# Optimization experiments

Measured on AMD Instinct MI355X. Metric: run time of the kernel, lower is better.

## Reference

```python
import jax, jax.numpy as jnp
from jax import lax
import numpy as np

# Quantization constants (would come from the torch state dict)
IN_S = 1.0 / 255.0   # input_scale
IN_ZP = 0            # input_zp
W_S  = [0.02, 0.02, 0.02, 0.02, 0.02, 0.02, 0.02]   # per-layer w_scale
W_ZP = [128, 128, 128, 128, 128, 128, 128]           # per-layer w_zp
OUT_S  = [0.05, 0.04, 0.04, 0.04, 0.04, 0.04, 0.05]  # per-layer act out_scale
OUT_ZP = [0, 0, 0, 0, 0, 0, 0]
PADS = [2, 0, 1, 1, 1, 1, 0]
WT_SCALE = 0.02  # last_part.w_scale used to dequantize the transpose-conv weight
DN = ('NCHW', 'OIHW', 'NCHW')


def qconv(x, w, b, in_s, in_zp, w_s, w_zp, out_s, out_zp, pad):
    # fake-quantize activation to uint8 range, shift by zero point
    xq = jnp.clip(jnp.round(x / in_s) + in_zp, 0.0, 255.0) - in_zp
    wq = w.astype(jnp.float32) - w_zp
    y = lax.conv_general_dilated(xq, wq, (1, 1), [(pad, pad), (pad, pad)],
                                 dimension_numbers=DN)
    y = y + b.astype(jnp.float32)[None, :, None, None]   # int32 accumulator bias
    # requantize to int8 range, dequantize, relu
    yq = jnp.clip(jnp.round(y * (in_s * w_s / out_s)), -127.0, 127.0)
    return jax.nn.relu((yq - out_zp) * out_s)


def deconv(x, wt):
    # torch ConvTranspose2d(16,1,k=9,stride=4,padding=4,bias=False)
    # equivalent: lhs-dilated conv with flipped, transposed kernel, pad = k-1-p = 4
    k = jnp.flip(jnp.transpose(wt, (1, 0, 2, 3)), axis=(2, 3))  # (O=1, I=16, 9, 9)
    return lax.conv_general_dilated(x, k, (1, 1), [(4, 4), (4, 4)],
                                    lhs_dilation=(4, 4), dimension_numbers=DN)


def setup_inputs() -> dict:
    key = jax.random.key(0)
    ks = jax.random.split(key, 20)
    shapes_w = [(16, 1, 5, 5), (12, 16, 1, 1), (12, 12, 3, 3), (12, 12, 3, 3),
                (12, 12, 3, 3), (12, 12, 3, 3), (16, 12, 1, 1)]
    inp = {"x": jax.random.uniform(ks[0], (16, 1, 512, 512), dtype=jnp.float32)}
    for i, sh in enumerate(shapes_w):
        inp[f"w{i}"] = jax.random.randint(ks[1 + i], sh, 0, 256, dtype=jnp.int32)
        inp[f"b{i}"] = jax.random.randint(ks[8 + i], (sh[0],), 0, 512, dtype=jnp.int32)
    # dequantized transpose-conv weight: int8-ish values * w_scale
    inp["wt"] = jax.random.normal(ks[15], (16, 1, 9, 9), dtype=jnp.float32) * WT_SCALE
    return inp


def reference(x, w0, w1, w2, w3, w4, w5, w6,
              b0, b1, b2, b3, b4, b5, b6, wt):
    ws = [w0, w1, w2, w3, w4, w5, w6]
    bs = [b0, b1, b2, b3, b4, b5, b6]
    cur_s, cur_zp = IN_S, IN_ZP
    for i in range(7):
        x = qconv(x, ws[i], bs[i], cur_s, cur_zp,
                  W_S[i], W_ZP[i], OUT_S[i], OUT_ZP[i], PADS[i])
        cur_s, cur_zp = OUT_S[i], OUT_ZP[i]
    return deconv(x, wt)
```

## Files before the change

### kernel.cpp

```cpp
#include <hip/hip_runtime.h>
#include <stdint.h>

typedef unsigned int uint;
typedef float f2 __attribute__((ext_vector_type(2)));
typedef float f4u __attribute__((ext_vector_type(4), aligned(4)));
#define DEV __device__ __forceinline__


DEV int dot4(uint a, uint b, int c) {
#if __has_builtin(__builtin_amdgcn_sdot4)
    return __builtin_amdgcn_sdot4((int)a, (int)b, c, false);
#else
    int r = c;
    r += (int)(int8_t)(a)       * (int)(int8_t)(b);
    r += (int)(int8_t)(a >> 8)  * (int)(int8_t)(b >> 8);
    r += (int)(int8_t)(a >> 16) * (int)(int8_t)(b >> 16);
    r += (int)(int8_t)(a >> 24) * (int)(int8_t)(b >> 24);
    return r;
#endif
}

DEV uint alignbyte(uint hi, uint lo, int m) {
#if __has_builtin(__builtin_amdgcn_alignbyte)
    return __builtin_amdgcn_alignbyte(hi, lo, m);
#else
    return (uint)((((uint64_t)hi << 32) | (uint64_t)lo) >> (8 * m));
#endif
}

DEV float bytef(uint v, int k) { return (float)((v >> (8 * k)) & 0xffu); }

DEV uint requant_relu(int acc, float M) {
    float q = rintf((float)acc * M);
    q = fminf(fmaxf(q, -127.f), 127.f);
    q = fmaxf(q, 0.f);
    return (uint)q;
}

__global__ __launch_bounds__(256) void k_quant(const float* __restrict__ x,
                                               uint8_t* __restrict__ xq,
                                               float in_s) {
    int i = blockIdx.x * 256 + threadIdx.x;
    float4 v = ((const float4*)x)[i];
    uint b0 = (uint)fminf(fmaxf(rintf(v.x / in_s), 0.f), 255.f);
    uint b1 = (uint)fminf(fmaxf(rintf(v.y / in_s), 0.f), 255.f);
    uint b2 = (uint)fminf(fmaxf(rintf(v.z / in_s), 0.f), 255.f);
    uint b3 = (uint)fminf(fmaxf(rintf(v.w / in_s), 0.f), 255.f);
    ((uint*)xq)[i] = b0 | (b1 << 8) | (b2 << 16) | (b3 << 24);
}

__global__ __launch_bounds__(256) void k_l0(const uint8_t* __restrict__ xq,
                                            const int* __restrict__ w,
                                            const int* __restrict__ b,
                                            uint8_t* __restrict__ out, float M,
                                            const int* __restrict__ w1,
                                            const int* __restrict__ b1, float M1) {
    __shared__ uint tin[5][68];
    __shared__ uint wrow[5][16];
    __shared__ uint w4p[16];
    __shared__ int  w44[16];
    __shared__ int  beff[16];
    __shared__ uint w1l[48];
    __shared__ int  b1l[12];
    int t  = threadIdx.x;
    int x0 = blockIdx.x * 256;
    int y  = blockIdx.y;
    int n  = blockIdx.z;
    const uint8_t* xp = xq + (size_t)n * 512 * 512;

    for (int j = t; j < 330; j += 256) {
        int r = j / 66, d = j % 66;
        int yy = y - 2 + r;
        int gb = x0 - 4 + 4 * d;
        uint v = 0;
        if ((unsigned)yy < 512u && (unsigned)gb < 512u)
            v = *(const uint*)(xp + (size_t)yy * 512 + gb);
        tin[r][d] = v;
    }
    if (t < 80) {
        int oc = t / 5, r = t % 5;
        uint pk = 0;
#pragma unroll
        for (int k = 0; k < 4; ++k) {
            int wv = w[oc * 25 + r * 5 + k] - 128;
            pk |= ((uint)(uint8_t)(int8_t)wv) << (8 * k);
        }
        wrow[r][oc] = pk;
    }
    if (t < 16) {
        uint pk = 0;
#pragma unroll
        for (int r = 0; r < 4; ++r) {
            int wv = w[t * 25 + r * 5 + 4] - 128;
            pk |= ((uint)(uint8_t)(int8_t)wv) << (8 * r);
        }
        w4p[t] = pk;
        w44[t] = w[t * 25 + 24] - 128;
        int s = 0;
        for (int p = 0; p < 25; ++p) s += w[t * 25 + p] - 128;
        beff[t] = b[t] + 128 * s;
    }
    if (t < 48) {
        int oc = t >> 2, d = t & 3;
        uint pk = 0;
#pragma unroll
        for (int k = 0; k < 4; ++k) {
            int wv = w1[oc * 16 + d * 4 + k] - 128;
            pk |= ((uint)(uint8_t)(int8_t)wv) << (8 * k);
        }
        w1l[t] = pk;
    }
    if (t >= 64 && t < 76) b1l[t - 64] = b1[t - 64];
    __syncthreads();

    int m  = (t + 2) & 3;
    int d0 = (t + 2) >> 2;
    uint e0[5], t4[5];
#pragma unroll
    for (int r = 0; r < 5; ++r) {
        uint a0 = tin[r][d0], a1 = tin[r][d0 + 1];
        e0[r] = alignbyte(a1, a0, m) ^ 0x80808080u;
        t4[r] = (a1 >> (8 * m)) & 0xffu;
    }
    uint lo4 = (t4[0] | (t4[1] << 8) | (t4[2] << 16) | (t4[3] << 24)) ^ 0x80808080u;
    int  e44 = (int)(int8_t)(uint8_t)(t4[4] ^ 0x80u);

    int acc[16];
#pragma unroll
    for (int oc = 0; oc < 16; ++oc) acc[oc] = beff[oc];
#pragma unroll
    for (int r = 0; r < 5; ++r)
#pragma unroll
        for (int oc = 0; oc < 16; ++oc) acc[oc] = dot4(e0[r], wrow[r][oc], acc[oc]);
#pragma unroll
    for (int oc = 0; oc < 16; ++oc) {
        acc[oc] = dot4(lo4, w4p[oc], acc[oc]);
        acc[oc] += e44 * w44[oc];
    }

    uint dw[4];
#pragma unroll
    for (int g = 0; g < 4; ++g) {
        uint d = 0;
#pragma unroll
        for (int k = 0; k < 4; ++k) d |= requant_relu(acc[g * 4 + k], M) << (8 * k);
        dw[g] = d;
    }

    size_t pix = (size_t)(n * 512 + y) * 512 + (x0 + t);
    uint* op = (uint*)out;
#pragma unroll
    for (int g = 0; g < 3; ++g) {
        uint dword = 0;
#pragma unroll
        for (int k = 0; k < 4; ++k) {
            int oc = g * 4 + k;
            int a2 = b1l[oc];
#pragma unroll
            for (int d = 0; d < 4; ++d) a2 = dot4(dw[d], w1l[oc * 4 + d], a2);
            dword |= requant_relu(a2, M1) << (8 * k);
        }
        op[pix * 3 + g] = dword;
    }
}

template <bool FUSE>
__global__ __launch_bounds__(128) void k_3x3(const uint8_t* __restrict__ in,
                                             const int* __restrict__ w,
                                             const int* __restrict__ b,
                                             uint8_t* __restrict__ out, float M,
                                             const int* __restrict__ w6,
                                             const int* __restrict__ b6, float M6) {
    __shared__ uint wl[324];
    __shared__ int  bl[12];
    __shared__ uint w6l[48];
    __shared__ int  b6l[16];
    int t = threadIdx.x;
    for (int j = t; j < 324; j += 128) {
        int pos = j / 36;
        int oc  = (j % 36) / 3;
        int d   = j % 3;
        uint pk = 0;
#pragma unroll
        for (int k = 0; k < 4; ++k) {
            int ic = d * 4 + k;
            int wv = w[oc * 108 + ic * 9 + pos] - 128;
            pk |= ((uint)(uint8_t)(int8_t)wv) << (8 * k);
        }
        wl[j] = pk;
    }
    if (t < 12) bl[t] = b[t];
    if (FUSE) {
        if (t >= 16 && t < 64) {
            int j = t - 16, oc = j / 3, d = j % 3;
            uint pk = 0;
#pragma unroll
            for (int k = 0; k < 4; ++k) {
                int wv = w6[oc * 12 + d * 4 + k] - 128;
                pk |= ((uint)(uint8_t)(int8_t)wv) << (8 * k);
            }
            w6l[j] = pk;
        }
        if (t >= 64 && t < 80) b6l[t - 64] = b6[t - 64];
    }
    __syncthreads();

    int y = blockIdx.x, n = blockIdx.y;
    int x0 = t * 4;
    const uint* ip = (const uint*)in;

    uint inr[3][6][3];
#pragma unroll
    for (int r = 0; r < 3; ++r) {
        int yy = y - 1 + r;
        bool yok = (unsigned)yy < 512u;
#pragma unroll
        for (int cidx = 0; cidx < 6; ++cidx) {
            int xx = x0 - 1 + cidx;
            bool ok = yok && (unsigned)xx < 512u;
            size_t base = ((size_t)(n * 512 + yy) * 512 + xx) * 3;
#pragma unroll
            for (int d = 0; d < 3; ++d) inr[r][cidx][d] = ok ? ip[base + d] : 0u;
        }
    }

    int acc[4][12];
#pragma unroll
    for (int p = 0; p < 4; ++p)
#pragma unroll
        for (int oc = 0; oc < 12; ++oc) acc[p][oc] = bl[oc];

#pragma unroll
    for (int ry = 0; ry < 3; ++ry) {
#pragma unroll
        for (int rx = 0; rx < 3; ++rx) {
            int pos = ry * 3 + rx;
            const uint4* wq = (const uint4*)&wl[pos * 36];
#pragma unroll
            for (int g = 0; g < 3; ++g) {
                uint4 wA = wq[g * 3 + 0];
                uint4 wB = wq[g * 3 + 1];
                uint4 wC = wq[g * 3 + 2];
                uint wocd[4][3] = {{wA.x, wA.y, wA.z}, {wA.w, wB.x, wB.y},
                                   {wB.z, wB.w, wC.x}, {wC.y, wC.z, wC.w}};
#pragma unroll
                for (int k = 0; k < 4; ++k) {
                    int oc = g * 4 + k;
#pragma unroll
                    for (int p = 0; p < 4; ++p) {
                        acc[p][oc] = dot4(inr[ry][rx + p][0], wocd[k][0], acc[p][oc]);
                        acc[p][oc] = dot4(inr[ry][rx + p][1], wocd[k][1], acc[p][oc]);
                        acc[p][oc] = dot4(inr[ry][rx + p][2], wocd[k][2], acc[p][oc]);
                    }
                }
            }
        }
    }

#pragma unroll
    for (int p = 0; p < 4; ++p) {
        uint dws[3];
#pragma unroll
        for (int g = 0; g < 3; ++g) {
            uint dword = 0;
#pragma unroll
            for (int k = 0; k < 4; ++k) dword |= requant_relu(acc[p][g * 4 + k], M) << (8 * k);
            dws[g] = dword;
        }
        size_t pix = (size_t)(n * 512 + y) * 512 + (x0 + p);
        if (!FUSE) {
            uint* op = (uint*)out;
            op[pix * 3 + 0] = dws[0];
            op[pix * 3 + 1] = dws[1];
            op[pix * 3 + 2] = dws[2];
        } else {
            uint dw2[4];
#pragma unroll
            for (int g = 0; g < 4; ++g) {
                uint dword = 0;
#pragma unroll
                for (int k = 0; k < 4; ++k) {
                    int oc = g * 4 + k;
                    int a2 = b6l[oc];
#pragma unroll
                    for (int d = 0; d < 3; ++d) a2 = dot4(dws[d], w6l[oc * 3 + d], a2);
                    dword |= requant_relu(a2, M6) << (8 * k);
                }
                dw2[g] = dword;
            }
            ((uint4*)out)[pix] = make_uint4(dw2[0], dw2[1], dw2[2], dw2[3]);
        }
    }
}

__global__ __launch_bounds__(256) void k_wprep(const float* __restrict__ wt,
                                               float* __restrict__ wp, float out_s) {
    int idx = blockIdx.x * 256 + threadIdx.x;
    if (idx < 2304) {
        int o = idx & 15, c = (idx >> 4) & 15, pos = idx >> 8;
        int r = pos / 3, s = pos % 3;
        int py = o >> 2, px = o & 3;
        int jy = 4 * r - py, jx = 4 * s - px;
        float v = 0.f;
        if (jy >= 0 && jy < 9 && jx >= 0 && jx < 9)
            v = wt[c * 81 + (8 - jy) * 9 + (8 - jx)] * out_s;
        wp[idx] = v;
    } else if (idx < 2496) {
        int i2 = idx - 2304;
        int r = i2 >> 6, c = (i2 >> 2) & 15, py = i2 & 3;
        int jy = 4 * r - py;
        float v = 0.f;
        if (jy >= 0 && jy < 9)
            v = wt[c * 81 + (8 - jy) * 9 + 8] * out_s;
        wp[idx] = v;
    }
}

template <bool ALLPY>
DEV void dc_row8(const float* __restrict__ wrow,
                 const float* __restrict__ w0tab,
                 const uint4* ld,
                 f2 (&accA)[2][4], f2 (&accB)[2][4]) {
    uint bv[4][4];
#pragma unroll
    for (int s = 0; s < 4; ++s) { bv[s][0] = ld[s].x; bv[s][1] = ld[s].y; bv[s][2] = ld[s].z; bv[s][3] = ld[s].w; }
#pragma unroll
    for (int c = 0; c < 16; ++c) {
        float xc[4];
#pragma unroll
        for (int s = 0; s < 4; ++s) xc[s] = bytef(bv[s][c >> 2], c & 3);
        if (ALLPY) {
            float4 wv = *(const float4*)(w0tab + c * 4);
            accA[0][0].x = fmaf(wv.x, xc[0], accA[0][0].x);
            accA[0][1].x = fmaf(wv.y, xc[0], accA[0][1].x);
            accA[0][2].x = fmaf(wv.z, xc[0], accA[0][2].x);
            accA[0][3].x = fmaf(wv.w, xc[0], accA[0][3].x);
            accA[1][0].x = fmaf(wv.x, xc[1], accA[1][0].x);
            accA[1][1].x = fmaf(wv.y, xc[1], accA[1][1].x);
            accA[1][2].x = fmaf(wv.z, xc[1], accA[1][2].x);
            accA[1][3].x = fmaf(wv.w, xc[1], accA[1][3].x);
        } else {
            float w0 = w0tab[c * 4];
            accA[0][0].x = fmaf(w0, xc[0], accA[0][0].x);
            accA[1][0].x = fmaf(w0, xc[1], accA[1][0].x);
        }
#pragma unroll
        for (int s = 1; s < 3; ++s) {
            const float* wb = wrow + s * 256 + c * 16;
            f2 xxA = {xc[s], xc[s]};
            f2 xxB = {xc[s + 1], xc[s + 1]};
#pragma unroll
            for (int py = 0; py < (ALLPY ? 4 : 1); ++py) {
                float4 wv = *(const float4*)(wb + py * 4);
                f2 wlo = {wv.x, wv.y};
                f2 whi = {wv.z, wv.w};
                accA[0][py] = __builtin_elementwise_fma(wlo, xxA, accA[0][py]);
                accB[0][py] = __builtin_elementwise_fma(whi, xxA, accB[0][py]);
                accA[1][py] = __builtin_elementwise_fma(wlo, xxB, accA[1][py]);
                accB[1][py] = __builtin_elementwise_fma(whi, xxB, accB[1][py]);
            }
        }
    }
}

__global__ __launch_bounds__(256, 2) void k_deconv8(const uint8_t* __restrict__ in,
                                                    const float* __restrict__ wp,
                                                    float* __restrict__ out) {
    __shared__ float wl[2304];
    __shared__ float wl0[192];
    int t = threadIdx.x;
#pragma unroll
    for (int j = 0; j < 9; ++j) wl[j * 256 + t] = wp[j * 256 + t];
    if (t < 192) wl0[t] = wp[2304 + t];
    __syncthreads();

    int gx = t;
    int ty = blockIdx.y;
    int n  = blockIdx.z;
    const uint4* ip = (const uint4*)in + (size_t)n * 512 * 512;

    f2 accA[2][4], accB[2][4];
#pragma unroll
    for (int k = 0; k < 2; ++k)
#pragma unroll
        for (int i = 0; i < 4; ++i) { accA[k][i] = (f2){0.f, 0.f}; accB[k][i] = (f2){0.f, 0.f}; }

    {
        int iy = ty - 1;
        uint4 ld[4];
#pragma unroll
        for (int s = 0; s < 4; ++s) {
            int ix = 2 * gx - 1 + s;
            bool ok = (iy >= 0) && ((unsigned)ix < 512u);
            ld[s] = ok ? ip[(size_t)iy * 512 + ix] : make_uint4(0u, 0u, 0u, 0u);
        }
        dc_row8<false>(&wl[0], &wl0[0], ld, accA, accB);
    }
#pragma unroll 1
    for (int r = 1; r < 3; ++r) {
        int iy = ty - 1 + r;
        uint4 ld[4];
#pragma unroll
        for (int s = 0; s < 4; ++s) {
            int ix = 2 * gx - 1 + s;
            bool ok = (iy < 512) && ((unsigned)ix < 512u);
            ld[s] = ok ? ip[(size_t)iy * 512 + ix] : make_uint4(0u, 0u, 0u, 0u);
        }
        dc_row8<true>(&wl[r * 768], &wl0[r * 64], ld, accA, accB);
    }

    int oy0 = 4 * ty, ox0 = 8 * gx;
    float* op = out + (size_t)n * 2045 * 2045;
#pragma unroll
    for (int py = 0; py < 4; ++py) {
        int oy = oy0 + py;
        if (oy >= 2045) break;
        size_t rb = (size_t)oy * 2045 + ox0;
        if (ox0 + 8 <= 2045) {
            f4u vA = {accA[0][py].x, accA[0][py].y, accB[0][py].x, accB[0][py].y};
            f4u vB = {accA[1][py].x, accA[1][py].y, accB[1][py].x, accB[1][py].y};
            *(f4u*)(op + rb)     = vA;
            *(f4u*)(op + rb + 4) = vB;
        } else {
            float va[8] = {accA[0][py].x, accA[0][py].y, accB[0][py].x, accB[0][py].y,
                           accA[1][py].x, accA[1][py].y, accB[1][py].x, accB[1][py].y};
            int xlim = 2045 - ox0;
#pragma unroll
            for (int px = 0; px < 8; ++px) {
                if (px >= xlim) break;
                op[rb + px] = va[px];
            }
        }
    }
}

extern "C" void kernel_launch(void* const* d_in, const int* in_sizes, int n_in,
                              void* d_out, int out_size, void* d_ws, size_t ws_size,
                              hipStream_t stream) {
    const float* x  = (const float*)d_in[0];
    const int*   w0 = (const int*)d_in[1];
    const int*   b0 = (const int*)d_in[2];
    const int*   w1 = (const int*)d_in[3];
    const int*   b1 = (const int*)d_in[4];
    const int*   w2 = (const int*)d_in[5];
    const int*   b2 = (const int*)d_in[6];
    const int*   w3 = (const int*)d_in[7];
    const int*   b3 = (const int*)d_in[8];
    const int*   w4 = (const int*)d_in[9];
    const int*   b4 = (const int*)d_in[10];
    const int*   w5 = (const int*)d_in[11];
    const int*   b5 = (const int*)d_in[12];
    const int*   w6 = (const int*)d_in[13];
    const int*   b6 = (const int*)d_in[14];
    const float* wt = (const float*)d_in[15];
    float* out = (float*)d_out;

    uint8_t* A  = (uint8_t*)d_ws;
    uint8_t* B  = (uint8_t*)d_ws + (size_t)(64 << 20);
    uint8_t* xq = B;
    float*  wpD = (float*)(B + (size_t)(60 << 20));

    const float M0  = (float)((1.0 / 255.0) * 0.02 / 0.05);
    const float M1  = (float)(0.05 * 0.02 / 0.04);
    const float M25 = (float)(0.04 * 0.02 / 0.04);
    const float M6  = (float)(0.04 * 0.02 / 0.05);
    const float IN_S_F = (float)(1.0 / 255.0);

    k_wprep<<<10, 256, 0, stream>>>(wt, wpD, 0.05f);
    k_quant<<<4096, 256, 0, stream>>>(x, xq, IN_S_F);
    k_l0<<<dim3(2, 512, 16), 256, 0, stream>>>(xq, w0, b0, A, M0, w1, b1, M1);
    k_3x3<false><<<dim3(512, 16), 128, 0, stream>>>(A, w2, b2, B, M25, nullptr, nullptr, 0.f);
    k_3x3<false><<<dim3(512, 16), 128, 0, stream>>>(B, w3, b3, A, M25, nullptr, nullptr, 0.f);
    k_3x3<false><<<dim3(512, 16), 128, 0, stream>>>(A, w4, b4, B, M25, nullptr, nullptr, 0.f);
    k_3x3<true><<<dim3(512, 16), 128, 0, stream>>>(B, w5, b5, A, M25, w6, b6, M6);
    k_deconv8<<<dim3(1, 512, 16), 256, 0, stream>>>(A, wpD, out);
}
```

Before: 511.8 us.

## Compute four output rows per 3x3 block with rolling row buffer

Each k_3x3 block now computes four consecutive output rows and keeps a rotating three-row register window, so each input row is loaded once per block instead of three times. Grid height drops to 128 and launch bounds request two blocks per SIMD. The aim is to cut redundant global and L2 traffic and per-block weight staging. The cost is more register pressure from three row buffers plus 48 accumulators, and far fewer blocks in the grid (2048), which may reduce latency hiding.

```diff
diff --git a/kernel.cpp b/kernel.cpp
--- a/kernel.cpp
+++ b/kernel.cpp
@@ -164,13 +164,97 @@
     }
 }
 
+
+#define ROW_LOAD(dst, yy) do {                                               \
+    int yy_ = (yy);                                                          \
+    bool yok_ = (unsigned)yy_ < 512u;                                        \
+    _Pragma("unroll")                                                        \
+    for (int ci = 0; ci < 6; ++ci) {                                         \
+        int xx_ = x0 - 1 + ci;                                               \
+        bool ok_ = yok_ && (unsigned)xx_ < 512u;                             \
+        size_t base_ = ((size_t)(n * 512 + yy_) * 512 + xx_) * 3;            \
+        _Pragma("unroll")                                                    \
+        for (int d = 0; d < 3; ++d) dst[ci][d] = ok_ ? ip[base_ + d] : 0u;   \
+    } } while (0)
+
+#define ACC_ROW(rowarr, ry) do {                                             \
+    _Pragma("unroll")                                                        \
+    for (int rx = 0; rx < 3; ++rx) {                                         \
+        int pos_ = (ry) * 3 + rx;                                            \
+        const uint4* wq_ = (const uint4*)&wl[pos_ * 36];                     \
+        _Pragma("unroll")                                                    \
+        for (int g = 0; g < 3; ++g) {                                        \
+            uint4 wA_ = wq_[g * 3 + 0];                                      \
+            uint4 wB_ = wq_[g * 3 + 1];                                      \
+            uint4 wC_ = wq_[g * 3 + 2];                                      \
+            uint wocd_[4][3] = {{wA_.x, wA_.y, wA_.z}, {wA_.w, wB_.x, wB_.y},\
+                                {wB_.z, wB_.w, wC_.x}, {wC_.y, wC_.z, wC_.w}};\
+            _Pragma("unroll")                                                \
+            for (int k = 0; k < 4; ++k) {                                    \
+                int oc_ = g * 4 + k;                                         \
+                _Pragma("unroll")                                            \
+                for (int p = 0; p < 4; ++p) {                                \
+                    acc[p][oc_] = dot4(rowarr[rx + p][0], wocd_[k][0], acc[p][oc_]); \
+                    acc[p][oc_] = dot4(rowarr[rx + p][1], wocd_[k][1], acc[p][oc_]); \
+                    acc[p][oc_] = dot4(rowarr[rx + p][2], wocd_[k][2], acc[p][oc_]); \
+                }                                                            \
+            }                                                                \
+        }                                                                    \
+    } } while (0)
+
+#define ACC_INIT() do {                                                      \
+    _Pragma("unroll")                                                        \
+    for (int p = 0; p < 4; ++p)                                              \
+        _Pragma("unroll")                                                    \
+        for (int oc = 0; oc < 12; ++oc) acc[p][oc] = bl[oc];                 \
+    } while (0)
+
+#define EPILOGUE(yout) do {                                                  \
+    int y_ = (yout);                                                         \
+    _Pragma("unroll")                                                        \
+    for (int p = 0; p < 4; ++p) {                                            \
+        uint dws_[3];                                                        \
+        _Pragma("unroll")                                                    \
+        for (int g = 0; g < 3; ++g) {                                        \
+            uint dword_ = 0;                                                 \
+            _Pragma("unroll")                                                \
+            for (int k = 0; k < 4; ++k)                                      \
+                dword_ |= requant_relu(acc[p][g * 4 + k], M) << (8 * k);     \
+            dws_[g] = dword_;                                                \
+        }                                                                    \
+        size_t pix_ = (size_t)(n * 512 + y_) * 512 + (x0 + p);               \
+        if (!FUSE) {                                                         \
+            uint* op_ = (uint*)out;                                          \
+            op_[pix_ * 3 + 0] = dws_[0];                                     \
+            op_[pix_ * 3 + 1] = dws_[1];                                     \
+            op_[pix_ * 3 + 2] = dws_[2];                                     \
+        } else {                                                             \
+            uint dw2_[4];                                                    \
+            _Pragma("unroll")                                                \
+            for (int g = 0; g < 4; ++g) {                                    \
+                uint dword_ = 0;                                             \
+                _Pragma("unroll")                                            \
+                for (int k = 0; k < 4; ++k) {                                \
+                    int oc_ = g * 4 + k;                                     \
+                    int a2_ = b6l[oc_];                                      \
+                    _Pragma("unroll")                                        \
+                    for (int d = 0; d < 3; ++d)                              \
+                        a2_ = dot4(dws_[d], w6l[oc_ * 3 + d], a2_);          \
+                    dword_ |= requant_relu(a2_, M6) << (8 * k);              \
+                }                                                            \
+                dw2_[g] = dword_;                                            \
+            }                                                                \
+            ((uint4*)out)[pix_] = make_uint4(dw2_[0], dw2_[1], dw2_[2], dw2_[3]); \
+        }                                                                    \
+    } } while (0)
+
 template <bool FUSE>
-__global__ __launch_bounds__(128) void k_3x3(const uint8_t* __restrict__ in,
-                                             const int* __restrict__ w,
-                                             const int* __restrict__ b,
-                                             uint8_t* __restrict__ out, float M,
-                                             const int* __restrict__ w6,
-                                             const int* __restrict__ b6, float M6) {
+__global__ __launch_bounds__(128, 2) void k_3x3(const uint8_t* __restrict__ in,
+                                                const int* __restrict__ w,
+                                                const int* __restrict__ b,
+                                                uint8_t* __restrict__ out, float M,
+                                                const int* __restrict__ w6,
+                                                const int* __restrict__ b6, float M6) {
     __shared__ uint wl[324];
     __shared__ int  bl[12];
     __shared__ uint w6l[48];
@@ -205,92 +289,23 @@
     }
     __syncthreads();
 
-    int y = blockIdx.x, n = blockIdx.y;
+    int y0 = blockIdx.x * 4, n = blockIdx.y;
     int x0 = t * 4;
     const uint* ip = (const uint*)in;
 
-    uint inr[3][6][3];
-#pragma unroll
-    for (int r = 0; r < 3; ++r) {
-        int yy = y - 1 + r;
-        bool yok = (unsigned)yy < 512u;
-#pragma unroll
-        for (int cidx = 0; cidx < 6; ++cidx) {
-            int xx = x0 - 1 + cidx;
-            bool ok = yok && (unsigned)xx < 512u;
-            size_t base = ((size_t)(n * 512 + yy) * 512 + xx) * 3;
-#pragma unroll
-            for (int d = 0; d < 3; ++d) inr[r][cidx][d] = ok ? ip[base + d] : 0u;
-        }
-    }
-
+    uint wa[6][3], wb[6][3], wc[6][3];
     int acc[4][12];
-#pragma unroll
-    for (int p = 0; p < 4; ++p)
-#pragma unroll
-        for (int oc = 0; oc < 12; ++oc) acc[p][oc] = bl[oc];
-
-#pragma unroll
-    for (int ry = 0; ry < 3; ++ry) {
-#pragma unroll
-        for (int rx = 0; rx < 3; ++rx) {
-            int pos = ry * 3 + rx;
-            const uint4* wq = (const uint4*)&wl[pos * 36];
-#pragma unroll
-            for (int g = 0; g < 3; ++g) {
-                uint4 wA = wq[g * 3 + 0];
-                uint4 wB = wq[g * 3 + 1];
-                uint4 wC = wq[g * 3 + 2];
-                uint wocd[4][3] = {{wA.x, wA.y, wA.z}, {wA.w, wB.x, wB.y},
-                                   {wB.z, wB.w, wC.x}, {wC.y, wC.z, wC.w}};
-#pragma unroll
-                for (int k = 0; k < 4; ++k) {
-                    int oc = g * 4 + k;
-#pragma unroll
-                    for (int p = 0; p < 4; ++p) {
-                        acc[p][oc] = dot4(inr[ry][rx + p][0], wocd[k][0], acc[p][oc]);
-                        acc[p][oc] = dot4(inr[ry][rx + p][1], wocd[k][1], acc[p][oc]);
-                        acc[p][oc] = dot4(inr[ry][rx + p][2], wocd[k][2], acc[p][oc]);
-                    }
-                }
-            }
-        }
-    }
-
-#pragma unroll
-    for (int p = 0; p < 4; ++p) {
-        uint dws[3];
-#pragma unroll
-        for (int g = 0; g < 3; ++g) {
-            uint dword = 0;
-#pragma unroll
-            for (int k = 0; k < 4; ++k) dword |= requant_relu(acc[p][g * 4 + k], M) << (8 * k);
-            dws[g] = dword;
-        }
-        size_t pix = (size_t)(n * 512 + y) * 512 + (x0 + p);
-        if (!FUSE) {
-            uint* op = (uint*)out;
-            op[pix * 3 + 0] = dws[0];
-            op[pix * 3 + 1] = dws[1];
-            op[pix * 3 + 2] = dws[2];
-        } else {
-            uint dw2[4];
-#pragma unroll
-            for (int g = 0; g < 4; ++g) {
-                uint dword = 0;
-#pragma unroll
-                for (int k = 0; k < 4; ++k) {
-                    int oc = g * 4 + k;
-                    int a2 = b6l[oc];
-#pragma unroll
-                    for (int d = 0; d < 3; ++d) a2 = dot4(dws[d], w6l[oc * 3 + d], a2);
-                    dword |= requant_relu(a2, M6) << (8 * k);
-                }
-                dw2[g] = dword;
-            }
-            ((uint4*)out)[pix] = make_uint4(dw2[0], dw2[1], dw2[2], dw2[3]);
-        }
-    }
+
+    ROW_LOAD(wa, y0 - 1);
+    ROW_LOAD(wb, y0);
+    ROW_LOAD(wc, y0 + 1);
+    ACC_INIT(); ACC_ROW(wa, 0); ACC_ROW(wb, 1); ACC_ROW(wc, 2); EPILOGUE(y0);
+    ROW_LOAD(wa, y0 + 2);
+    ACC_INIT(); ACC_ROW(wb, 0); ACC_ROW(wc, 1); ACC_ROW(wa, 2); EPILOGUE(y0 + 1);
+    ROW_LOAD(wb, y0 + 3);
+    ACC_INIT(); ACC_ROW(wc, 0); ACC_ROW(wa, 1); ACC_ROW(wb, 2); EPILOGUE(y0 + 2);
+    ROW_LOAD(wc, y0 + 4);
+    ACC_INIT(); ACC_ROW(wa, 0); ACC_ROW(wb, 1); ACC_ROW(wc, 2); EPILOGUE(y0 + 3);
 }
 
 __global__ __launch_bounds__(256) void k_wprep(const float* __restrict__ wt,
@@ -469,9 +484,9 @@
     k_wprep<<<10, 256, 0, stream>>>(wt, wpD, 0.05f);
     k_quant<<<4096, 256, 0, stream>>>(x, xq, IN_S_F);
     k_l0<<<dim3(2, 512, 16), 256, 0, stream>>>(xq, w0, b0, A, M0, w1, b1, M1);
-    k_3x3<false><<<dim3(512, 16), 128, 0, stream>>>(A, w2, b2, B, M25, nullptr, nullptr, 0.f);
-    k_3x3<false><<<dim3(512, 16), 128, 0, stream>>>(B, w3, b3, A, M25, nullptr, nullptr, 0.f);
-    k_3x3<false><<<dim3(512, 16), 128, 0, stream>>>(A, w4, b4, B, M25, nullptr, nullptr, 0.f);
-    k_3x3<true><<<dim3(512, 16), 128, 0, stream>>>(B, w5, b5, A, M25, w6, b6, M6);
+    k_3x3<false><<<dim3(128, 16), 128, 0, stream>>>(A, w2, b2, B, M25, nullptr, nullptr, 0.f);
+    k_3x3<false><<<dim3(128, 16), 128, 0, stream>>>(B, w3, b3, A, M25, nullptr, nullptr, 0.f);
+    k_3x3<false><<<dim3(128, 16), 128, 0, stream>>>(A, w4, b4, B, M25, nullptr, nullptr, 0.f);
+    k_3x3<true><<<dim3(128, 16), 128, 0, stream>>>(B, w5, b5, A, M25, w6, b6, M6);
     k_deconv8<<<dim3(1, 512, 16), 256, 0, stream>>>(A, wpD, out);
 }
```

Result: faster. 494.7 us (median of 2 runs) (-3.4%).
